# Performance work log

Hardware: AMD Instinct MI355X
Metric: run time of the kernel (lower is better)

The kernel has to match this reference:

```python
import jax, jax.numpy as jnp
import numpy as np

NUM_CLASSES = 512  # label_id values are in [0, NUM_CLASSES)
MARGIN = 1.0
EPS = 1e-6  # torch F.pairwise_distance default eps, added to the difference


def setup_inputs() -> dict:
    key = jax.random.key(0)
    k1, k2 = jax.random.split(key)
    N, D = 65536, 512
    output = jax.random.normal(k1, (N, D), dtype=jnp.float32)
    label_id = jax.random.randint(k2, (N,), 0, NUM_CLASSES, dtype=jnp.int64)
    return {"output": output, "label_id": label_id}


def reference(output, label_id):
    # Note: in the original torch code pre_class is never updated, so the
    # branch fires for EVERY sample i: per-sample class mean and
    # complement-class mean are gathered, giving [N, D] matrices.
    n = output.shape[0]
    # Per-class sums and counts in one segment-reduce pass.
    cls_sums = jax.ops.segment_sum(output, label_id, num_segments=NUM_CLASSES)      # [C, D]
    cls_cnts = jax.ops.segment_sum(jnp.ones((n,), output.dtype), label_id,
                                   num_segments=NUM_CLASSES)                        # [C]
    total = jnp.sum(output, axis=0)                                                 # [D]
    # Gather per-sample class stats (every present class has count >= 1).
    s = cls_sums[label_id]                 # [N, D] sum of own class
    c = cls_cnts[label_id][:, None]        # [N, 1] count of own class
    mu_pos = s / c                         # mean of samples with same label
    mu_neg = (total - s) / (n - c)         # mean of samples with different label
    # F.pairwise_distance(x, y) = || x - y + eps ||_2
    d = jnp.sqrt(jnp.sum((mu_pos - mu_neg + EPS) ** 2, axis=-1, keepdims=True))  # [N, 1]
    return jnp.mean(jnp.maximum(MARGIN - d, 0.0) ** 2)
```

## Files before the change

### kernel.cpp

```cpp
#include <hip/hip_runtime.h>

#define NCLS 512
#define DIM 512
#define D4 128
#define EPS 1e-6f
#define MARGIN 1.0f

__global__ __launch_bounds__(512)
void k_init(int* __restrict__ cnts)
{
    cnts[threadIdx.x] = 0;
}

__global__ __launch_bounds__(256)
void k_hist(const int* __restrict__ lab, int* __restrict__ cnts, int N)
{
    __shared__ int h[NCLS];
    const int t = threadIdx.x;
    h[t] = 0; h[t + 256] = 0;
    __syncthreads();

    const int4* lab4 = (const int4*)lab;
    const int nv = N >> 2;
    for (int j = blockIdx.x * 256 + t; j < nv; j += gridDim.x * 256) {
        const int4 l = lab4[j];
        atomicAdd(&h[l.x], 1);
        atomicAdd(&h[l.y], 1);
        atomicAdd(&h[l.z], 1);
        atomicAdd(&h[l.w], 1);
    }
    __syncthreads();
    if (h[t])       atomicAdd(&cnts[t], h[t]);
    if (h[t + 256]) atomicAdd(&cnts[t + 256], h[t + 256]);
}

__global__ __launch_bounds__(512)
void k_scan(const int* __restrict__ cnts, int* __restrict__ offsets,
            int* __restrict__ cur, float* __restrict__ d_out)
{
    __shared__ int h[NCLS];
    const int t = threadIdx.x;
    const int myc = cnts[t];
    h[t] = myc;
    __syncthreads();
    for (int o = 1; o < NCLS; o <<= 1) {
        const int add = (t >= o) ? h[t - o] : 0;
        __syncthreads();
        h[t] += add;
        __syncthreads();
    }
    offsets[t] = h[t] - myc;
    cur[t]     = h[t] - myc;
    if (t == 0) d_out[0] = 0.f;
}

__global__ __launch_bounds__(256)
void k_scatter(const int* __restrict__ lab, int* __restrict__ cur,
               int* __restrict__ sorted, int N)
{
    int i = blockIdx.x * blockDim.x + threadIdx.x;
    const int stride = gridDim.x * blockDim.x;
    for (; i < N; i += stride) {
        const int c = lab[i];
        const int p = atomicAdd(&cur[c], 1);
        sorted[p] = i;
    }
}

__global__ __launch_bounds__(512)
void k_gather(const float4* __restrict__ x4, const int* __restrict__ sorted,
              const int* __restrict__ offsets, const int* __restrict__ cnts,
              float4* __restrict__ cls_sums4)
{
    const int c    = blockIdx.x;
    const int t    = threadIdx.x;
    const int col4 = t & 127;
    const int rq   = t >> 7;
    const int off  = offsets[c];
    const int cnt  = cnts[c];

    __shared__ int    s_idx[512];
    __shared__ float4 s_red[512];

    float4 acc = make_float4(0.f, 0.f, 0.f, 0.f);

    for (int done = 0; done < cnt; done += 512) {
        const int chunk = min(cnt - done, 512);
        if (t < chunk) s_idx[t] = sorted[off + done + t];
        __syncthreads();

        int base = 0;
        for (; base + 16 <= chunk; base += 16) {
            const int i0 = s_idx[base + rq];
            const int i1 = s_idx[base + 4 + rq];
            const int i2 = s_idx[base + 8 + rq];
            const int i3 = s_idx[base + 12 + rq];
            const float4 v0 = x4[(size_t)i0 * D4 + col4];
            const float4 v1 = x4[(size_t)i1 * D4 + col4];
            const float4 v2 = x4[(size_t)i2 * D4 + col4];
            const float4 v3 = x4[(size_t)i3 * D4 + col4];
            acc.x += (v0.x + v1.x) + (v2.x + v3.x);
            acc.y += (v0.y + v1.y) + (v2.y + v3.y);
            acc.z += (v0.z + v1.z) + (v2.z + v3.z);
            acc.w += (v0.w + v1.w) + (v2.w + v3.w);
        }
        for (; base + rq < chunk; base += 4) {
            const int i = s_idx[base + rq];
            const float4 v = x4[(size_t)i * D4 + col4];
            acc.x += v.x; acc.y += v.y; acc.z += v.z; acc.w += v.w;
        }
        __syncthreads();
    }

    s_red[t] = acc;
    __syncthreads();
    if (t < 128) {
        float4 s = s_red[t];
        const float4 a = s_red[t + 128];
        const float4 b = s_red[t + 256];
        const float4 d = s_red[t + 384];
        s.x += (a.x + b.x) + d.x;
        s.y += (a.y + b.y) + d.y;
        s.z += (a.z + b.z) + d.z;
        s.w += (a.w + b.w) + d.w;
        cls_sums4[(size_t)c * D4 + t] = s;
    }
}

__global__ __launch_bounds__(128)
void k_total(const float4* __restrict__ cls_sums4, float4* __restrict__ total4)
{
    const int col4 = blockIdx.x * 32 + (threadIdx.x & 31);
    const int cg   = threadIdx.x >> 5;
    float4 s = make_float4(0.f, 0.f, 0.f, 0.f);
    for (int c = cg * 128; c < cg * 128 + 128; c += 4) {
        const float4 a = cls_sums4[(size_t)(c + 0) * D4 + col4];
        const float4 b = cls_sums4[(size_t)(c + 1) * D4 + col4];
        const float4 d = cls_sums4[(size_t)(c + 2) * D4 + col4];
        const float4 e = cls_sums4[(size_t)(c + 3) * D4 + col4];
        s.x += (a.x + b.x) + (d.x + e.x);
        s.y += (a.y + b.y) + (d.y + e.y);
        s.z += (a.z + b.z) + (d.z + e.z);
        s.w += (a.w + b.w) + (d.w + e.w);
    }
    __shared__ float4 red[128];
    red[threadIdx.x] = s;
    __syncthreads();
    if (threadIdx.x < 32) {
        float4 a = red[threadIdx.x];
        const float4 b = red[threadIdx.x + 32];
        const float4 d = red[threadIdx.x + 64];
        const float4 e = red[threadIdx.x + 96];
        a.x += (b.x + d.x) + e.x;
        a.y += (b.y + d.y) + e.y;
        a.z += (b.z + d.z) + e.z;
        a.w += (b.w + d.w) + e.w;
        total4[col4] = a;
    }
}

__global__ __launch_bounds__(256)
void k_finalize(const float* __restrict__ cls_sums, const int* __restrict__ cnts,
                const float* __restrict__ total, float* __restrict__ d_out, int N)
{
    const int c   = blockIdx.x;
    const int tid = threadIdx.x;
    const int cnt = cnts[c];

    const float2 s = ((const float2*)cls_sums)[c * (DIM / 2) + tid];
    const float2 t = ((const float2*)total)[tid];

    float ss = 0.f;
    if (cnt > 0) {
        const float inv_c  = 1.f / (float)cnt;
        const float inv_nc = 1.f / (float)(N - cnt);
        const float d0 = s.x * inv_c - (t.x - s.x) * inv_nc + EPS;
        const float d1 = s.y * inv_c - (t.y - s.y) * inv_nc + EPS;
        ss = d0 * d0 + d1 * d1;
    }

    #pragma unroll
    for (int o = 1; o < 64; o <<= 1) ss += __shfl_xor(ss, o, 64);

    __shared__ float s_red[4];
    if ((tid & 63) == 0) s_red[tid >> 6] = ss;
    __syncthreads();

    if (tid == 0) {
        const float tot = (s_red[0] + s_red[1]) + (s_red[2] + s_red[3]);
        const float d = sqrtf(tot);
        const float w = fmaxf(MARGIN - d, 0.f);
        if (cnt > 0) atomicAdd(d_out, (float)cnt * w * w / (float)N);
    }
}

extern "C" void kernel_launch(void* const* d_in, const int* in_sizes, int n_in,
                              void* d_out, int out_size, void* d_ws, size_t ws_size,
                              hipStream_t stream)
{
    const float* x   = (const float*)d_in[0];
    const int*   lab = (const int*)d_in[1];
    float*       out = (float*)d_out;

    const int N = in_sizes[1];

    float* cls_sums = (float*)d_ws;
    float* total    = cls_sums + (size_t)NCLS * DIM;
    int*   cnts     = (int*)(total + DIM);
    int*   offsets  = cnts + NCLS;
    int*   cur      = offsets + NCLS;
    int*   sorted   = cur + NCLS;

    k_init<<<1, 512, 0, stream>>>(cnts);
    k_hist<<<64, 256, 0, stream>>>(lab, cnts, N);
    k_scan<<<1, 512, 0, stream>>>(cnts, offsets, cur, out);
    k_scatter<<<64, 256, 0, stream>>>(lab, cur, sorted, N);
    k_gather<<<NCLS, 512, 0, stream>>>((const float4*)x, sorted, offsets, cnts,
                                       (float4*)cls_sums);
    k_total<<<4, 128, 0, stream>>>((const float4*)cls_sums, (float4*)total);
    k_finalize<<<NCLS, 256, 0, stream>>>(cls_sums, cnts, total, out, N);
}
```

Before: 73.04 us.

## Split class gather across two blocks and drop histogram init kernel

The gather kernel now runs two blocks per class, each summing half of the class's samples into separate partial-sum buffers. Finalize and total combine the two halves. The histogram writes per-block partials that the scan kernel reduces, which removes the init kernel and the global atomics. Scatter and total get wider grids. This targets under-occupancy of the 512-block gather on a large GPU, at the cost of an extra launch-free partial buffer and more workspace traffic.

```diff
diff --git a/kernel.cpp b/kernel.cpp
--- a/kernel.cpp
+++ b/kernel.cpp
@@ -3,26 +3,24 @@
 #define NCLS 512
 #define DIM 512
 #define D4 128
+#define NHB 16
 #define EPS 1e-6f
 #define MARGIN 1.0f
 
-__global__ __launch_bounds__(512)
-void k_init(int* __restrict__ cnts)
-{
-    cnts[threadIdx.x] = 0;
-}
-
-__global__ __launch_bounds__(256)
-void k_hist(const int* __restrict__ lab, int* __restrict__ cnts, int N)
+__global__ __launch_bounds__(256)
+void k_hist(const int* __restrict__ lab, int* __restrict__ hist_part, int N)
 {
     __shared__ int h[NCLS];
     const int t = threadIdx.x;
+    const int b = blockIdx.x;
     h[t] = 0; h[t + 256] = 0;
     __syncthreads();
 
     const int4* lab4 = (const int4*)lab;
     const int nv = N >> 2;
-    for (int j = blockIdx.x * 256 + t; j < nv; j += gridDim.x * 256) {
+    const int per = nv / NHB;
+    const int j0 = b * per;
+    for (int j = j0 + t; j < j0 + per; j += 256) {
         const int4 l = lab4[j];
         atomicAdd(&h[l.x], 1);
         atomicAdd(&h[l.y], 1);
@@ -30,17 +28,20 @@
         atomicAdd(&h[l.w], 1);
     }
     __syncthreads();
-    if (h[t])       atomicAdd(&cnts[t], h[t]);
-    if (h[t + 256]) atomicAdd(&cnts[t + 256], h[t + 256]);
+    hist_part[b * NCLS + t]       = h[t];
+    hist_part[b * NCLS + t + 256] = h[t + 256];
 }
 
 __global__ __launch_bounds__(512)
-void k_scan(const int* __restrict__ cnts, int* __restrict__ offsets,
-            int* __restrict__ cur, float* __restrict__ d_out)
+void k_scan(const int* __restrict__ hist_part, int* __restrict__ cnts,
+            int* __restrict__ offsets, int* __restrict__ cur, float* __restrict__ d_out)
 {
     __shared__ int h[NCLS];
     const int t = threadIdx.x;
-    const int myc = cnts[t];
+    int myc = 0;
+    #pragma unroll
+    for (int b = 0; b < NHB; ++b) myc += hist_part[b * NCLS + t];
+    cnts[t] = myc;
     h[t] = myc;
     __syncthreads();
     for (int o = 1; o < NCLS; o <<= 1) {
@@ -70,23 +71,29 @@
 __global__ __launch_bounds__(512)
 void k_gather(const float4* __restrict__ x4, const int* __restrict__ sorted,
               const int* __restrict__ offsets, const int* __restrict__ cnts,
-              float4* __restrict__ cls_sums4)
-{
-    const int c    = blockIdx.x;
+              float4* __restrict__ cls_part4)
+{
+    const int c    = blockIdx.x >> 1;
+    const int p    = blockIdx.x & 1;
     const int t    = threadIdx.x;
     const int col4 = t & 127;
     const int rq   = t >> 7;
     const int off  = offsets[c];
     const int cnt  = cnts[c];
+    const int half = (cnt + 1) >> 1;
+    const int start = off + p * half;
+    int m = cnt - p * half;
+    if (m > half) m = half;
+    if (m < 0)    m = 0;
 
     __shared__ int    s_idx[512];
     __shared__ float4 s_red[512];
 
     float4 acc = make_float4(0.f, 0.f, 0.f, 0.f);
 
-    for (int done = 0; done < cnt; done += 512) {
-        const int chunk = min(cnt - done, 512);
-        if (t < chunk) s_idx[t] = sorted[off + done + t];
+    for (int done = 0; done < m; done += 512) {
+        const int chunk = min(m - done, 512);
+        if (t < chunk) s_idx[t] = sorted[start + done + t];
         __syncthreads();
 
         int base = 0;
@@ -123,59 +130,55 @@
         s.y += (a.y + b.y) + d.y;
         s.z += (a.z + b.z) + d.z;
         s.w += (a.w + b.w) + d.w;
-        cls_sums4[(size_t)c * D4 + t] = s;
-    }
-}
-
-__global__ __launch_bounds__(128)
-void k_total(const float4* __restrict__ cls_sums4, float4* __restrict__ total4)
-{
-    const int col4 = blockIdx.x * 32 + (threadIdx.x & 31);
-    const int cg   = threadIdx.x >> 5;
+        cls_part4[((size_t)p * NCLS + c) * D4 + t] = s;
+    }
+}
+
+__global__ __launch_bounds__(256)
+void k_total(const float4* __restrict__ cls_part4, float4* __restrict__ total4)
+{
+    const int t    = threadIdx.x;
+    const int col4 = blockIdx.x * 8 + (t & 7);
+    const int g    = t >> 3;
     float4 s = make_float4(0.f, 0.f, 0.f, 0.f);
-    for (int c = cg * 128; c < cg * 128 + 128; c += 4) {
-        const float4 a = cls_sums4[(size_t)(c + 0) * D4 + col4];
-        const float4 b = cls_sums4[(size_t)(c + 1) * D4 + col4];
-        const float4 d = cls_sums4[(size_t)(c + 2) * D4 + col4];
-        const float4 e = cls_sums4[(size_t)(c + 3) * D4 + col4];
-        s.x += (a.x + b.x) + (d.x + e.x);
-        s.y += (a.y + b.y) + (d.y + e.y);
-        s.z += (a.z + b.z) + (d.z + e.z);
-        s.w += (a.w + b.w) + (d.w + e.w);
-    }
-    __shared__ float4 red[128];
-    red[threadIdx.x] = s;
-    __syncthreads();
-    if (threadIdx.x < 32) {
-        float4 a = red[threadIdx.x];
-        const float4 b = red[threadIdx.x + 32];
-        const float4 d = red[threadIdx.x + 64];
-        const float4 e = red[threadIdx.x + 96];
-        a.x += (b.x + d.x) + e.x;
-        a.y += (b.y + d.y) + e.y;
-        a.z += (b.z + d.z) + e.z;
-        a.w += (b.w + d.w) + e.w;
+    for (int r = g; r < 2 * NCLS; r += 32) {
+        const float4 v = cls_part4[(size_t)r * D4 + col4];
+        s.x += v.x; s.y += v.y; s.z += v.z; s.w += v.w;
+    }
+    __shared__ float4 red[256];
+    red[t] = s;
+    __syncthreads();
+    if (t < 8) {
+        float4 a = red[t];
+        #pragma unroll
+        for (int k = 1; k < 32; ++k) {
+            const float4 b = red[t + 8 * k];
+            a.x += b.x; a.y += b.y; a.z += b.z; a.w += b.w;
+        }
         total4[col4] = a;
     }
 }
 
 __global__ __launch_bounds__(256)
-void k_finalize(const float* __restrict__ cls_sums, const int* __restrict__ cnts,
+void k_finalize(const float* __restrict__ cls_part, const int* __restrict__ cnts,
                 const float* __restrict__ total, float* __restrict__ d_out, int N)
 {
     const int c   = blockIdx.x;
     const int tid = threadIdx.x;
     const int cnt = cnts[c];
 
-    const float2 s = ((const float2*)cls_sums)[c * (DIM / 2) + tid];
-    const float2 t = ((const float2*)total)[tid];
+    const float2 s0 = ((const float2*)cls_part)[c * (DIM / 2) + tid];
+    const float2 s1 = ((const float2*)cls_part)[(NCLS + c) * (DIM / 2) + tid];
+    const float2 t  = ((const float2*)total)[tid];
+    const float sx = s0.x + s1.x;
+    const float sy = s0.y + s1.y;
 
     float ss = 0.f;
     if (cnt > 0) {
         const float inv_c  = 1.f / (float)cnt;
         const float inv_nc = 1.f / (float)(N - cnt);
-        const float d0 = s.x * inv_c - (t.x - s.x) * inv_nc + EPS;
-        const float d1 = s.y * inv_c - (t.y - s.y) * inv_nc + EPS;
+        const float d0 = sx * inv_c - (t.x - sx) * inv_nc + EPS;
+        const float d1 = sy * inv_c - (t.y - sy) * inv_nc + EPS;
         ss = d0 * d0 + d1 * d1;
     }
 
@@ -204,19 +207,19 @@
 
     const int N = in_sizes[1];
 
-    float* cls_sums = (float*)d_ws;
-    float* total    = cls_sums + (size_t)NCLS * DIM;
-    int*   cnts     = (int*)(total + DIM);
-    int*   offsets  = cnts + NCLS;
-    int*   cur      = offsets + NCLS;
-    int*   sorted   = cur + NCLS;
-
-    k_init<<<1, 512, 0, stream>>>(cnts);
-    k_hist<<<64, 256, 0, stream>>>(lab, cnts, N);
-    k_scan<<<1, 512, 0, stream>>>(cnts, offsets, cur, out);
-    k_scatter<<<64, 256, 0, stream>>>(lab, cur, sorted, N);
-    k_gather<<<NCLS, 512, 0, stream>>>((const float4*)x, sorted, offsets, cnts,
-                                       (float4*)cls_sums);
-    k_total<<<4, 128, 0, stream>>>((const float4*)cls_sums, (float4*)total);
-    k_finalize<<<NCLS, 256, 0, stream>>>(cls_sums, cnts, total, out, N);
-}
+    float* cls_part  = (float*)d_ws;
+    float* total     = cls_part + (size_t)2 * NCLS * DIM;
+    int*   cnts      = (int*)(total + DIM);
+    int*   offsets   = cnts + NCLS;
+    int*   cur       = offsets + NCLS;
+    int*   hist_part = cur + NCLS;
+    int*   sorted    = hist_part + NHB * NCLS;
+
+    k_hist    <<<NHB, 256, 0, stream>>>(lab, hist_part, N);
+    k_scan    <<<1, 512, 0, stream>>>(hist_part, cnts, offsets, cur, out);
+    k_scatter <<<128, 256, 0, stream>>>(lab, cur, sorted, N);
+    k_gather  <<<2 * NCLS, 512, 0, stream>>>((const float4*)x, sorted, offsets, cnts,
+                                             (float4*)cls_part);
+    k_total   <<<16, 256, 0, stream>>>((const float4*)cls_part, (float4*)total);
+    k_finalize<<<NCLS, 256, 0, stream>>>(cls_part, cnts, total, out, N);
+}
```

After: 76.66 us. +5.0%, slower.
